# Performance work log

Measured on AMD Instinct MI355X. Metric: run time of the kernel, lower is better.

Reference implementation:

```python
import jax, jax.numpy as jnp
import numpy as np

B, N, H = 8, 128, 768      # batch, words, BERT hidden
HID, L = 384, 100          # MLP hidden, label_num


def setup_inputs() -> dict:
    key = jax.random.key(0)
    k0, k1, k2 = jax.random.split(key, 3)
    s = 0.02
    return {
        "repr_w": jax.random.normal(k0, (B, N, H), jnp.float32),
        "W1": jax.random.normal(k1, (2 * H, HID), jnp.float32) * s,
        "b1": jnp.zeros((HID,), jnp.float32),
        "W2": jax.random.normal(k2, (HID, L), jnp.float32) * s,
        "b2": jnp.zeros((L,), jnp.float32),
    }


def reference(repr_w, W1, b1, W2, b2):
    # Original: table[b,i,j] = concat(repr_w[b,j] (row_h), repr_w[b,i] (column_h))
    # then MLP: relu(table @ W1 + b1) @ W2 + b2  (dropout inactive in eval).
    # Decompose the concat-GEMM: concat(r_j, r_i) @ W1 == r_j @ W1[:H] + r_i @ W1[H:].
    W1_row, W1_col = W1[:H], W1[H:]
    p = jnp.einsum('bnh,hd->bnd', repr_w, W1_row)  # contribution indexed by j
    q = jnp.einsum('bnh,hd->bnd', repr_w, W1_col)  # contribution indexed by i
    h = jax.nn.relu(p[:, None, :, :] + q[:, :, None, :] + b1)  # [B,N,N,HID]
    return jnp.einsum('bijd,dl->bijl', h, W2) + b2              # [B,N,N,L]
```

## Files before the change

kernel.cpp:

```cpp
#include <hip/hip_runtime.h>
#include <hip/hip_bf16.h>

#define B_   8
#define N_   128
#define H_   768
#define HID_ 384
#define L_   100

typedef float f32x4 __attribute__((ext_vector_type(4)));
typedef short s16x8 __attribute__((ext_vector_type(8)));

__device__ __forceinline__ short f2bf(float f) {
    __hip_bfloat16 h = __float2bfloat16(f);
    return __builtin_bit_cast(short, h);
}

__global__ void prep_w1f(const float* __restrict__ W1, short* __restrict__ W1f) {
    int tid = blockIdx.x * 256 + threadIdx.x;
    if (tid >= 48 * 24 * 64) return;
    int lane = tid & 63;
    int kk   = (tid >> 6) % 24;
    int ct   = tid / (24 * 64);
    int c    = ct * 16 + (lane & 15);
    int k0   = kk * 32 + ((lane >> 4) << 3);
    short v[8];
#pragma unroll
    for (int e = 0; e < 8; ++e) {
        int k = k0 + e;
        float f = (c < HID_) ? W1[(size_t)k * HID_ + c]
                             : W1[(size_t)(H_ + k) * HID_ + (c - HID_)];
        v[e] = f2bf(f);
    }
    ((s16x8*)W1f)[tid] = *(const s16x8*)v;
}

__global__ void prep_w2f(const float* __restrict__ W2, short* __restrict__ W2f) {
    int tid = blockIdx.x * 256 + threadIdx.x;
    if (tid >= 12 * 7 * 64) return;
    int lane = tid & 63;
    int t    = (tid >> 6) % 7;
    int kk   = tid / (7 * 64);
    int c    = t * 16 + (lane & 15);
    int k0   = kk * 32 + ((lane >> 4) << 3);
    short v[8];
#pragma unroll
    for (int e = 0; e < 8; ++e) {
        float f = (c < L_) ? W2[(size_t)(k0 + e) * L_ + c] : 0.0f;
        v[e] = f2bf(f);
    }
    ((s16x8*)W2f)[tid] = *(const s16x8*)v;
}

__global__ __launch_bounds__(256) void pq_gemm(
    const float* __restrict__ repr, const short* __restrict__ W1f,
    const float* __restrict__ b1,
    float* __restrict__ P, float* __restrict__ Q)
{
    const int wid  = blockIdx.x * 4 + (threadIdx.x >> 6);
    const int lane = threadIdx.x & 63;
    const int l15  = lane & 15;
    const int g    = lane >> 4;
    const int rt   = wid / 12;
    const int cg   = wid % 12;

    f32x4 acc[4];
#pragma unroll
    for (int n = 0; n < 4; ++n) { acc[n][0]=0.f; acc[n][1]=0.f; acc[n][2]=0.f; acc[n][3]=0.f; }

    const float* aptr  = repr + (size_t)(rt * 16 + l15) * H_ + (g << 3);
    const s16x8* bbase = (const s16x8*)W1f + (size_t)(cg * 4) * 24 * 64 + lane;

    for (int kk = 0; kk < 24; ++kk) {
        float a[8];
        *(float4*)&a[0] = *(const float4*)(aptr + kk * 32);
        *(float4*)&a[4] = *(const float4*)(aptr + kk * 32 + 4);
        s16x8 af;
#pragma unroll
        for (int e = 0; e < 8; ++e) af[e] = f2bf(a[e]);
#pragma unroll
        for (int n = 0; n < 4; ++n) {
            s16x8 bf = bbase[(size_t)(n * 24 + kk) * 64];
            acc[n] = __builtin_amdgcn_mfma_f32_16x16x32_bf16(af, bf, acc[n], 0, 0, 0);
        }
    }

    const int r0 = rt * 16 + (g << 2);
#pragma unroll
    for (int n = 0; n < 4; ++n) {
        int c = (cg * 4 + n) * 16 + l15;
#pragma unroll
        for (int r = 0; r < 4; ++r) {
            float v = acc[n][r];
            int row = r0 + r;
            if (c < HID_) P[(size_t)row * HID_ + c] = v + b1[c];
            else          Q[(size_t)row * HID_ + (c - HID_)] = v;
        }
    }
}

__global__ __launch_bounds__(256, 2) void fused_out(
    const float* __restrict__ P, const float* __restrict__ Q,
    const short* __restrict__ W2f, const float* __restrict__ b2,
    float* __restrict__ out)
{
    const int blk  = blockIdx.x;
    const int b    = blk >> 6;
    const int i0   = (blk & 63) << 1;
    const int w    = threadIdx.x >> 6;
    const int lane = threadIdx.x & 63;
    const int l15  = lane & 15;
    const int g    = lane >> 4;
    const int j0   = w << 5;

    const float* __restrict__ Pb = P + (size_t)(b * N_) * HID_;
    const float* __restrict__ Q0 = Q + (size_t)(b * N_ + i0) * HID_;

    f32x4 acc[2][2][7];
#pragma unroll
    for (int ii = 0; ii < 2; ++ii)
#pragma unroll
        for (int jt = 0; jt < 2; ++jt)
#pragma unroll
            for (int t = 0; t < 7; ++t) {
                acc[ii][jt][t][0]=0.f; acc[ii][jt][t][1]=0.f;
                acc[ii][jt][t][2]=0.f; acc[ii][jt][t][3]=0.f;
            }

    const float* prow0 = Pb + (size_t)(j0 + l15) * HID_;
    const float* prow1 = Pb + (size_t)(j0 + 16 + l15) * HID_;

    for (int kk = 0; kk < 12; ++kk) {
        const int d0 = kk * 32 + (g << 3);

        float q0[8], q1[8], p0[8], p1[8];
        *(float4*)&q0[0] = *(const float4*)(Q0 + d0);
        *(float4*)&q0[4] = *(const float4*)(Q0 + d0 + 4);
        *(float4*)&q1[0] = *(const float4*)(Q0 + HID_ + d0);
        *(float4*)&q1[4] = *(const float4*)(Q0 + HID_ + d0 + 4);
        *(float4*)&p0[0] = *(const float4*)(prow0 + d0);
        *(float4*)&p0[4] = *(const float4*)(prow0 + d0 + 4);
        *(float4*)&p1[0] = *(const float4*)(prow1 + d0);
        *(float4*)&p1[4] = *(const float4*)(prow1 + d0 + 4);

        s16x8 af[2][2];
#pragma unroll
        for (int e = 0; e < 8; ++e) {
            af[0][0][e] = f2bf(fmaxf(p0[e] + q0[e], 0.f));
            af[0][1][e] = f2bf(fmaxf(p1[e] + q0[e], 0.f));
            af[1][0][e] = f2bf(fmaxf(p0[e] + q1[e], 0.f));
            af[1][1][e] = f2bf(fmaxf(p1[e] + q1[e], 0.f));
        }

        const s16x8* bfp = (const s16x8*)W2f + (size_t)(kk * 7) * 64 + lane;
#pragma unroll
        for (int t = 0; t < 7; ++t) {
            s16x8 bf = bfp[(size_t)t * 64];
#pragma unroll
            for (int ii = 0; ii < 2; ++ii)
#pragma unroll
                for (int jt = 0; jt < 2; ++jt)
                    acc[ii][jt][t] = __builtin_amdgcn_mfma_f32_16x16x32_bf16(
                        af[ii][jt], bf, acc[ii][jt][t], 0, 0, 0);
        }
    }

    float bias[7];
#pragma unroll
    for (int t = 0; t < 7; ++t) {
        int l = t * 16 + l15;
        bias[t] = (l < L_) ? b2[l] : 0.f;
    }

#pragma unroll
    for (int ii = 0; ii < 2; ++ii) {
        const size_t obase = (size_t)(b * N_ + (i0 + ii)) * N_ * L_;
#pragma unroll
        for (int jt = 0; jt < 2; ++jt) {
#pragma unroll
            for (int r = 0; r < 4; ++r) {
                int j = j0 + jt * 16 + (g << 2) + r;
                float* op = out + obase + (size_t)j * L_;
#pragma unroll
                for (int t = 0; t < 7; ++t) {
                    int l = t * 16 + l15;
                    if (l < L_) op[l] = acc[ii][jt][t][r] + bias[t];
                }
            }
        }
    }
}

extern "C" void kernel_launch(void* const* d_in, const int* in_sizes, int n_in,
                              void* d_out, int out_size, void* d_ws, size_t ws_size,
                              hipStream_t stream)
{
    const float* repr = (const float*)d_in[0];
    const float* W1   = (const float*)d_in[1];
    const float* b1   = (const float*)d_in[2];
    const float* W2   = (const float*)d_in[3];
    const float* b2   = (const float*)d_in[4];
    float* out = (float*)d_out;

    char* ws = (char*)d_ws;
    float* P   = (float*)(ws);
    float* Qm  = (float*)(ws + 1572864);
    short* W1f = (short*)(ws + 3145728);
    short* W2f = (short*)(ws + 3145728 + 1179648);

    hipLaunchKernelGGL(prep_w1f, dim3(288), dim3(256), 0, stream, W1, W1f);
    hipLaunchKernelGGL(prep_w2f, dim3(21),  dim3(256), 0, stream, W2, W2f);
    hipLaunchKernelGGL(pq_gemm,  dim3(192), dim3(256), 0, stream, repr, W1f, b1, P, Qm);
    hipLaunchKernelGGL(fused_out, dim3(512), dim3(256), 0, stream, P, Qm, W2f, b2, out);
}
```

Measured before the change: 132.1 us.

## Shrink per-wave tiles to raise parallelism and prefetch P/Q in fused kernel

pq_gemm now gives each wave a single 16-column tile, and its grid grows from 192 to 768 blocks. fused_out splits the j dimension into halves, so each wave handles 16 j rows instead of 32. That doubles the grid to 1024 blocks and raises the occupancy hint to 4 blocks per CU. The K loop is unrolled, the next P/Q slice is register-prefetched, and output stores become nontemporal. The aim is to fill more CUs and hide load latency, at the cost of less reuse of each W2 fragment and Q load per wave.

```diff
diff --git a/kernel.cpp b/kernel.cpp
--- a/kernel.cpp
+++ b/kernel.cpp
@@ -56,20 +56,21 @@
     const float* __restrict__ b1,
     float* __restrict__ P, float* __restrict__ Q)
 {
-    const int wid  = blockIdx.x * 4 + (threadIdx.x >> 6);
+    const int blk  = blockIdx.x;
+    const int rt   = blk / 12;
+    const int w    = threadIdx.x >> 6;
+    const int ct   = (blk % 12) * 4 + w;
     const int lane = threadIdx.x & 63;
     const int l15  = lane & 15;
     const int g    = lane >> 4;
-    const int rt   = wid / 12;
-    const int cg   = wid % 12;
-
-    f32x4 acc[4];
-#pragma unroll
-    for (int n = 0; n < 4; ++n) { acc[n][0]=0.f; acc[n][1]=0.f; acc[n][2]=0.f; acc[n][3]=0.f; }
+
+    f32x4 acc;
+    acc[0] = 0.f; acc[1] = 0.f; acc[2] = 0.f; acc[3] = 0.f;
 
     const float* aptr  = repr + (size_t)(rt * 16 + l15) * H_ + (g << 3);
-    const s16x8* bbase = (const s16x8*)W1f + (size_t)(cg * 4) * 24 * 64 + lane;
-
+    const s16x8* bbase = (const s16x8*)W1f + (size_t)(ct * 24) * 64 + lane;
+
+#pragma unroll 4
     for (int kk = 0; kk < 24; ++kk) {
         float a[8];
         *(float4*)&a[0] = *(const float4*)(aptr + kk * 32);
@@ -77,90 +78,87 @@
         s16x8 af;
 #pragma unroll
         for (int e = 0; e < 8; ++e) af[e] = f2bf(a[e]);
-#pragma unroll
-        for (int n = 0; n < 4; ++n) {
-            s16x8 bf = bbase[(size_t)(n * 24 + kk) * 64];
-            acc[n] = __builtin_amdgcn_mfma_f32_16x16x32_bf16(af, bf, acc[n], 0, 0, 0);
-        }
+        s16x8 bf = bbase[(size_t)kk * 64];
+        acc = __builtin_amdgcn_mfma_f32_16x16x32_bf16(af, bf, acc, 0, 0, 0);
     }
 
     const int r0 = rt * 16 + (g << 2);
-#pragma unroll
-    for (int n = 0; n < 4; ++n) {
-        int c = (cg * 4 + n) * 16 + l15;
-#pragma unroll
-        for (int r = 0; r < 4; ++r) {
-            float v = acc[n][r];
-            int row = r0 + r;
-            if (c < HID_) P[(size_t)row * HID_ + c] = v + b1[c];
-            else          Q[(size_t)row * HID_ + (c - HID_)] = v;
-        }
-    }
-}
-
-__global__ __launch_bounds__(256, 2) void fused_out(
+    const int c  = ct * 16 + l15;
+#pragma unroll
+    for (int r = 0; r < 4; ++r) {
+        int row = r0 + r;
+        float v = acc[r];
+        if (c < HID_) P[(size_t)row * HID_ + c] = v + b1[c];
+        else          Q[(size_t)row * HID_ + (c - HID_)] = v;
+    }
+}
+
+__global__ __launch_bounds__(256, 4) void fused_out(
     const float* __restrict__ P, const float* __restrict__ Q,
     const short* __restrict__ W2f, const float* __restrict__ b2,
     float* __restrict__ out)
 {
     const int blk  = blockIdx.x;
-    const int b    = blk >> 6;
-    const int i0   = (blk & 63) << 1;
+    const int b    = blk >> 7;
+    const int rem  = blk & 127;
+    const int i0   = (rem >> 1) << 1;
+    const int jh   = rem & 1;
     const int w    = threadIdx.x >> 6;
     const int lane = threadIdx.x & 63;
     const int l15  = lane & 15;
     const int g    = lane >> 4;
-    const int j0   = w << 5;
-
-    const float* __restrict__ Pb = P + (size_t)(b * N_) * HID_;
-    const float* __restrict__ Q0 = Q + (size_t)(b * N_ + i0) * HID_;
-
-    f32x4 acc[2][2][7];
+    const int j0   = jh * 64 + w * 16;
+
+    const float* __restrict__ prow = P + ((size_t)(b * N_) + j0 + l15) * HID_ + (g << 3);
+    const float* __restrict__ q0p  = Q + (size_t)(b * N_ + i0) * HID_ + (g << 3);
+    const float* __restrict__ q1p  = q0p + HID_;
+
+    f32x4 acc[2][7];
 #pragma unroll
     for (int ii = 0; ii < 2; ++ii)
 #pragma unroll
-        for (int jt = 0; jt < 2; ++jt)
-#pragma unroll
-            for (int t = 0; t < 7; ++t) {
-                acc[ii][jt][t][0]=0.f; acc[ii][jt][t][1]=0.f;
-                acc[ii][jt][t][2]=0.f; acc[ii][jt][t][3]=0.f;
-            }
-
-    const float* prow0 = Pb + (size_t)(j0 + l15) * HID_;
-    const float* prow1 = Pb + (size_t)(j0 + 16 + l15) * HID_;
-
+        for (int t = 0; t < 7; ++t) {
+            acc[ii][t][0] = 0.f; acc[ii][t][1] = 0.f;
+            acc[ii][t][2] = 0.f; acc[ii][t][3] = 0.f;
+        }
+
+    float4 lp0  = *(const float4*)(prow);
+    float4 lp1  = *(const float4*)(prow + 4);
+    float4 lq00 = *(const float4*)(q0p);
+    float4 lq01 = *(const float4*)(q0p + 4);
+    float4 lq10 = *(const float4*)(q1p);
+    float4 lq11 = *(const float4*)(q1p + 4);
+
+#pragma unroll
     for (int kk = 0; kk < 12; ++kk) {
-        const int d0 = kk * 32 + (g << 3);
-
-        float q0[8], q1[8], p0[8], p1[8];
-        *(float4*)&q0[0] = *(const float4*)(Q0 + d0);
-        *(float4*)&q0[4] = *(const float4*)(Q0 + d0 + 4);
-        *(float4*)&q1[0] = *(const float4*)(Q0 + HID_ + d0);
-        *(float4*)&q1[4] = *(const float4*)(Q0 + HID_ + d0 + 4);
-        *(float4*)&p0[0] = *(const float4*)(prow0 + d0);
-        *(float4*)&p0[4] = *(const float4*)(prow0 + d0 + 4);
-        *(float4*)&p1[0] = *(const float4*)(prow1 + d0);
-        *(float4*)&p1[4] = *(const float4*)(prow1 + d0 + 4);
-
-        s16x8 af[2][2];
+        float p[8], q0v[8], q1v[8];
+        *(float4*)&p[0]   = lp0;  *(float4*)&p[4]   = lp1;
+        *(float4*)&q0v[0] = lq00; *(float4*)&q0v[4] = lq01;
+        *(float4*)&q1v[0] = lq10; *(float4*)&q1v[4] = lq11;
+
+        if (kk < 11) {
+            const int d = (kk + 1) * 32;
+            lp0  = *(const float4*)(prow + d);
+            lp1  = *(const float4*)(prow + d + 4);
+            lq00 = *(const float4*)(q0p + d);
+            lq01 = *(const float4*)(q0p + d + 4);
+            lq10 = *(const float4*)(q1p + d);
+            lq11 = *(const float4*)(q1p + d + 4);
+        }
+
+        s16x8 af0, af1;
 #pragma unroll
         for (int e = 0; e < 8; ++e) {
-            af[0][0][e] = f2bf(fmaxf(p0[e] + q0[e], 0.f));
-            af[0][1][e] = f2bf(fmaxf(p1[e] + q0[e], 0.f));
-            af[1][0][e] = f2bf(fmaxf(p0[e] + q1[e], 0.f));
-            af[1][1][e] = f2bf(fmaxf(p1[e] + q1[e], 0.f));
+            af0[e] = f2bf(fmaxf(p[e] + q0v[e], 0.f));
+            af1[e] = f2bf(fmaxf(p[e] + q1v[e], 0.f));
         }
 
         const s16x8* bfp = (const s16x8*)W2f + (size_t)(kk * 7) * 64 + lane;
 #pragma unroll
         for (int t = 0; t < 7; ++t) {
             s16x8 bf = bfp[(size_t)t * 64];
-#pragma unroll
-            for (int ii = 0; ii < 2; ++ii)
-#pragma unroll
-                for (int jt = 0; jt < 2; ++jt)
-                    acc[ii][jt][t] = __builtin_amdgcn_mfma_f32_16x16x32_bf16(
-                        af[ii][jt], bf, acc[ii][jt][t], 0, 0, 0);
+            acc[0][t] = __builtin_amdgcn_mfma_f32_16x16x32_bf16(af0, bf, acc[0][t], 0, 0, 0);
+            acc[1][t] = __builtin_amdgcn_mfma_f32_16x16x32_bf16(af1, bf, acc[1][t], 0, 0, 0);
         }
     }
 
@@ -175,16 +173,13 @@
     for (int ii = 0; ii < 2; ++ii) {
         const size_t obase = (size_t)(b * N_ + (i0 + ii)) * N_ * L_;
 #pragma unroll
-        for (int jt = 0; jt < 2; ++jt) {
-#pragma unroll
-            for (int r = 0; r < 4; ++r) {
-                int j = j0 + jt * 16 + (g << 2) + r;
-                float* op = out + obase + (size_t)j * L_;
-#pragma unroll
-                for (int t = 0; t < 7; ++t) {
-                    int l = t * 16 + l15;
-                    if (l < L_) op[l] = acc[ii][jt][t][r] + bias[t];
-                }
+        for (int r = 0; r < 4; ++r) {
+            int j = j0 + (g << 2) + r;
+            float* op = out + obase + (size_t)j * L_;
+#pragma unroll
+            for (int t = 0; t < 7; ++t) {
+                int l = t * 16 + l15;
+                if (l < L_) __builtin_nontemporal_store(acc[ii][t][r] + bias[t], op + l);
             }
         }
     }
@@ -207,8 +202,8 @@
     short* W1f = (short*)(ws + 3145728);
     short* W2f = (short*)(ws + 3145728 + 1179648);
 
-    hipLaunchKernelGGL(prep_w1f, dim3(288), dim3(256), 0, stream, W1, W1f);
-    hipLaunchKernelGGL(prep_w2f, dim3(21),  dim3(256), 0, stream, W2, W2f);
-    hipLaunchKernelGGL(pq_gemm,  dim3(192), dim3(256), 0, stream, repr, W1f, b1, P, Qm);
-    hipLaunchKernelGGL(fused_out, dim3(512), dim3(256), 0, stream, P, Qm, W2f, b2, out);
-}
+    hipLaunchKernelGGL(prep_w1f,  dim3(288),  dim3(256), 0, stream, W1, W1f);
+    hipLaunchKernelGGL(prep_w2f,  dim3(21),   dim3(256), 0, stream, W2, W2f);
+    hipLaunchKernelGGL(pq_gemm,   dim3(768),  dim3(256), 0, stream, repr, W1f, b1, P, Qm);
+    hipLaunchKernelGGL(fused_out, dim3(1024), dim3(256), 0, stream, P, Qm, W2f, b2, out);
+}
```

Result: slower. 147.5 us (+11.7%).
